# Performance work log

Hardware: AMD Instinct MI355X
Metric: run time of the kernel (lower is better)

The kernel has to match this reference:

```python
import jax, jax.numpy as jnp
import numpy as np

N_NODES = 50000
N_EDGES = 1600000


def _gcn_conv(x, src, dst, W, b, num_nodes):
    # PyG GCNConv: out = D^-1/2 (A + I) D^-1/2 (x W) + b
    h = x @ W  # transform first (in_channels >= out_channels)
    deg = jax.ops.segment_sum(jnp.ones_like(dst, dtype=h.dtype), dst,
                              num_segments=num_nodes)
    dinv = jax.lax.rsqrt(deg)  # deg >= 1 thanks to self-loops
    norm = dinv[src] * dinv[dst]  # [E+N]
    msg = h[src] * norm[:, None]  # gather + scale
    out = jax.ops.segment_sum(msg, dst, num_segments=num_nodes)
    return out + b


def setup_inputs() -> dict:
    key = jax.random.key(0)
    k1, k2, k3, k4 = jax.random.split(key, 4)
    x = jax.random.normal(k1, (N_NODES, 512), dtype=jnp.float32)
    edge_index = jax.random.randint(k2, (2, N_EDGES), 0, N_NODES, dtype=jnp.int64)
    # Glorot-ish init for the two GCNConv weights
    W1 = jax.random.normal(k3, (512, 128), dtype=jnp.float32) * (1.0 / np.sqrt(512))
    b1 = jnp.zeros((128,), dtype=jnp.float32)
    W2 = jax.random.normal(k4, (128, 64), dtype=jnp.float32) * (1.0 / np.sqrt(128))
    b2 = jnp.zeros((64,), dtype=jnp.float32)
    return {"x": x, "edge_index": edge_index, "W1": W1, "b1": b1,
            "W2": W2, "b2": b2}


def reference(x, edge_index, W1, b1, W2, b2):
    num_nodes = x.shape[0]
    loop = jnp.arange(num_nodes, dtype=edge_index.dtype)
    src = jnp.concatenate([edge_index[0], loop])  # add self-loops
    dst = jnp.concatenate([edge_index[1], loop])
    h = jax.nn.relu(_gcn_conv(x, src, dst, W1, b1, num_nodes))
    out = _gcn_conv(h, src, dst, W2, b2, num_nodes)
    return out
```

## Files before the change

### kernel.cpp

```cpp
#include <hip/hip_runtime.h>
#include <hip/hip_bf16.h>


typedef __attribute__((ext_vector_type(8))) short short8;
typedef __attribute__((ext_vector_type(4))) float f32x4;

#define BSHIFT 9
#define BSIZE 512
constexpr int NBMAX = 128;
constexpr int CAP = 32768;
constexpr int CHUNK = 4096;

__device__ __forceinline__ unsigned short bf16_bits(float f) {
  __hip_bfloat16 h = __float2bfloat16(f);
  return *(unsigned short*)&h;
}
__device__ __forceinline__ float bf16_f(unsigned short u) {
  __hip_bfloat16 h = *(__hip_bfloat16*)&u;
  return __bfloat162float(h);
}

__device__ __forceinline__ void gload_lds16(const void* g, void* l) {
  __builtin_amdgcn_global_load_lds(
      (const __attribute__((address_space(1))) unsigned*)g,
      (__attribute__((address_space(3))) unsigned*)l, 16, 0, 0);
}

__device__ __forceinline__ int edge_at(const void* p, long long i, int is64) {
  return is64 ? (int)((const long long*)p)[i] : ((const int*)p)[i];
}

__global__ void k_detect(const int* __restrict__ w, int* flag, int nwords,
                         int* __restrict__ ccur, int NB) {
  __shared__ int nz;
  if (threadIdx.x == 0) nz = 0;
  __syncthreads();
  for (int i = 1 + 2 * (int)threadIdx.x; i < nwords; i += 2 * (int)blockDim.x)
    if (w[i] != 0) nz = 1;
  if ((int)threadIdx.x < NB) ccur[threadIdx.x] = (int)threadIdx.x * CAP;
  __syncthreads();
  if (threadIdx.x == 0) *flag = (nz == 0) ? 1 : 0;
}

__global__ __launch_bounds__(256) void k_binA(
    const void* __restrict__ eidx, const int* __restrict__ flag,
    int* __restrict__ ccur, unsigned* __restrict__ pairs, int E, int NB) {
  __shared__ int cnt[NBMAX];
  __shared__ int scn[NBMAX + 1];
  __shared__ int cur[NBMAX];
  __shared__ int gbase[NBMAX];
  __shared__ unsigned out[CHUNK];
  const int is64 = *flag;
  const int tid = threadIdx.x;
  const int cs = blockIdx.x * CHUNK;
  const int n = min(CHUNK, E - cs);
  for (int b = tid; b < NB; b += 256) cnt[b] = 0;
  __syncthreads();
  unsigned pk[CHUNK / 256];
#pragma unroll
  for (int it = 0; it < CHUNK / 256; ++it) {
    int i = cs + it * 256 + tid;
    unsigned p = 0xFFFFFFFFu;
    if (i < E) {
      int s = edge_at(eidx, i, is64);
      int d = edge_at(eidx, (long long)E + i, is64);
      p = ((unsigned)d << 16) | (unsigned)s;
      atomicAdd(&cnt[d >> BSHIFT], 1);
    }
    pk[it] = p;
  }
  __syncthreads();
  if (tid < NB) scn[tid + 1] = cnt[tid];
  if (tid == 0) scn[0] = 0;
  __syncthreads();
  for (int off = 1; off < NB; off <<= 1) {
    int t = 0;
    if (tid < NB && tid + 1 > off) t = scn[tid + 1 - off];
    __syncthreads();
    if (tid < NB && tid + 1 > off) scn[tid + 1] += t;
    __syncthreads();
  }
  if (tid < NB) {
    cur[tid] = scn[tid];
    gbase[tid] = (cnt[tid] > 0) ? atomicAdd(&ccur[tid], cnt[tid]) : 0;
  }
  __syncthreads();
#pragma unroll
  for (int it = 0; it < CHUNK / 256; ++it) {
    unsigned p = pk[it];
    if (p != 0xFFFFFFFFu) {
      int b = (int)(p >> (16 + BSHIFT));
      int pos = atomicAdd(&cur[b], 1);
      out[pos] = p;
    }
  }
  __syncthreads();
  for (int p2 = tid; p2 < n; p2 += 256) {
    unsigned v = out[p2];
    int b = (int)(v >> (16 + BSHIFT));
    pairs[gbase[b] + (p2 - scn[b])] = v;
  }
}

__global__ __launch_bounds__(128) void k_scanb(
    const int* __restrict__ ccur, int* __restrict__ bbase,
    int* __restrict__ rowptr, int NB, int N, int E) {
  __shared__ int buf[NBMAX];
  int tid = threadIdx.x;
  int v = (tid < NB) ? (ccur[tid] - tid * CAP) : 0;
  buf[tid] = v;
  __syncthreads();
  for (int off = 1; off < NBMAX; off <<= 1) {
    int t = (tid >= off) ? buf[tid - off] : 0;
    __syncthreads();
    buf[tid] += t;
    __syncthreads();
  }
  if (tid < NB) bbase[tid] = buf[tid] - v;
  if (tid == 0) rowptr[N] = E;
}

__global__ __launch_bounds__(256) void k_binB(
    const unsigned* __restrict__ pairs, const int* __restrict__ ccur,
    const int* __restrict__ bbase, int* __restrict__ rowptr,
    float* __restrict__ dinv, int* __restrict__ elist, int N) {
  __shared__ int hist[BSIZE];
  __shared__ int loc[BSIZE];
  const int b = blockIdx.x;
  const int tid = threadIdx.x;
  const int nbeg = b * CAP;
  const int cntb = ccur[b] - nbeg;
  const int base = bbase[b];
  const int j0 = tid, j1 = tid + 256;
  hist[j0] = 0; hist[j1] = 0;
  __syncthreads();
  for (int i = tid; i < cntb; i += 256) {
    unsigned v = pairs[nbeg + i];
    atomicAdd(&hist[(v >> 16) & (BSIZE - 1)], 1);
  }
  __syncthreads();
  loc[j0] = hist[j0]; loc[j1] = hist[j1];
  __syncthreads();
  for (int off = 1; off < BSIZE; off <<= 1) {
    int v0 = (j0 >= off) ? loc[j0 - off] : 0;
    int v1 = (j1 >= off) ? loc[j1 - off] : 0;
    __syncthreads();
    loc[j0] += v0; loc[j1] += v1;
    __syncthreads();
  }
  int c0 = base + loc[j0] - hist[j0];
  int c1 = base + loc[j1] - hist[j1];
  int gd0 = b * BSIZE + j0, gd1 = b * BSIZE + j1;
  if (gd0 < N) { rowptr[gd0] = c0; dinv[gd0] = rsqrtf((float)(hist[j0] + 1)); }
  if (gd1 < N) { rowptr[gd1] = c1; dinv[gd1] = rsqrtf((float)(hist[j1] + 1)); }
  __syncthreads();
  hist[j0] = c0; hist[j1] = c1;
  __syncthreads();
  for (int i = tid; i < cntb; i += 256) {
    unsigned v = pairs[nbeg + i];
    int p = atomicAdd(&hist[(v >> 16) & (BSIZE - 1)], 1);
    elist[p] = (int)(v & 0xFFFFu);
  }
}

__global__ void k_prepw(const float* __restrict__ W, unsigned short* __restrict__ Whi,
                        unsigned short* __restrict__ Wlo, int K, int N) {
  int o = blockIdx.x * blockDim.x + threadIdx.x;
  if (o >= K * N) return;
  int n = o / K, k = o % K;
  float w = W[(long long)k * N + n];
  unsigned short hb = bf16_bits(w);
  unsigned short lb = bf16_bits(w - bf16_f(hb));
  Whi[o] = hb;
  Wlo[o] = lb;
}

template <int K, int NOUT, int WM, int WY, int WX>
__global__ __launch_bounds__(256) void k_gemm_mfma(
    const float* __restrict__ X, const unsigned short* __restrict__ Whi,
    const unsigned short* __restrict__ Wlo, const float* __restrict__ dinv,
    unsigned short* __restrict__ Hs, int M) {
  constexpr int BM = WM * WY;
  constexpr int BN = 64 * WX;
  constexpr int KC = 32;
  constexpr int I = WM / 16;
  static_assert(WY * WX == 4, "4 waves");
  static_assert(BN == NOUT, "block covers full N");
  static_assert((BN * 4) % 256 == 0, "B chunk count divisible by block");
  __shared__ unsigned short Ah[BM][KC], Al[BM][KC];
  __shared__ unsigned short Bh[BN][KC], Bl[BN][KC];
  const int tid = threadIdx.x;
  const int lane = tid & 63, wv = tid >> 6;
  const int wy = wv / WX, wx = wv % WX;
  const int fm = lane & 15;
  const int fq = lane >> 4;
  const int base = blockIdx.x * BM;

  f32x4 acc[I][4];
#pragma unroll
  for (int i = 0; i < I; ++i)
#pragma unroll
    for (int j = 0; j < 4; ++j) acc[i][j] = (f32x4){0.f, 0.f, 0.f, 0.f};

  for (int k0 = 0; k0 < K; k0 += KC) {
    __syncthreads();
#pragma unroll
    for (int it = 0; it < BM / 32; ++it) {
      int chunk = tid + it * 256;
      int r = chunk >> 3, c = chunk & 7;
      float4 v = make_float4(0.f, 0.f, 0.f, 0.f);
      if (base + r < M) v = *(const float4*)&X[(long long)(base + r) * K + k0 + c * 4];
      ushort4 hv, lv;
      hv.x = bf16_bits(v.x); lv.x = bf16_bits(v.x - bf16_f(hv.x));
      hv.y = bf16_bits(v.y); lv.y = bf16_bits(v.y - bf16_f(hv.y));
      hv.z = bf16_bits(v.z); lv.z = bf16_bits(v.z - bf16_f(hv.z));
      hv.w = bf16_bits(v.w); lv.w = bf16_bits(v.w - bf16_f(hv.w));
      *(ushort4*)&Ah[r][c * 4] = hv;
      *(ushort4*)&Al[r][c * 4] = lv;
    }
#pragma unroll
    for (int it = 0; it < (BN * 4) / 256; ++it) {
      int cb = it * 256 + wv * 64;
      int chunk = cb + lane;
      int n = chunk >> 2, cc = chunk & 3;
      const long long go = (long long)n * K + k0 + cc * 8;
      gload_lds16(&Whi[go], (unsigned short*)Bh + (size_t)cb * 8);
      gload_lds16(&Wlo[go], (unsigned short*)Bl + (size_t)cb * 8);
    }
    __syncthreads();
    short8 ah[I], al[I], bh[4], bl[4];
#pragma unroll
    for (int i = 0; i < I; ++i) {
      ah[i] = *(short8*)&Ah[wy * WM + i * 16 + fm][fq * 8];
      al[i] = *(short8*)&Al[wy * WM + i * 16 + fm][fq * 8];
    }
#pragma unroll
    for (int j = 0; j < 4; ++j) {
      bh[j] = *(short8*)&Bh[wx * 64 + j * 16 + fm][fq * 8];
      bl[j] = *(short8*)&Bl[wx * 64 + j * 16 + fm][fq * 8];
    }
#pragma unroll
    for (int i = 0; i < I; ++i)
#pragma unroll
      for (int j = 0; j < 4; ++j) {
        acc[i][j] = __builtin_amdgcn_mfma_f32_16x16x32_bf16(ah[i], bh[j], acc[i][j], 0, 0, 0);
        acc[i][j] = __builtin_amdgcn_mfma_f32_16x16x32_bf16(ah[i], bl[j], acc[i][j], 0, 0, 0);
        acc[i][j] = __builtin_amdgcn_mfma_f32_16x16x32_bf16(al[i], bh[j], acc[i][j], 0, 0, 0);
      }
  }
#pragma unroll
  for (int i = 0; i < I; ++i) {
#pragma unroll
    for (int reg = 0; reg < 4; ++reg) {
      int row = base + wy * WM + i * 16 + fq * 4 + reg;
      if (row < M) {
        float dv = dinv[row];
#pragma unroll
        for (int j = 0; j < 4; ++j)
          Hs[(long long)row * NOUT + wx * 64 + j * 16 + fm] =
              bf16_bits(acc[i][j][reg] * dv);
      }
    }
  }
}

__device__ __forceinline__ void acc8(float* a, uint4 u) {
  const unsigned* p = (const unsigned*)&u;
#pragma unroll
  for (int q = 0; q < 4; ++q) {
    unsigned w = p[q];
    a[2 * q]     += __uint_as_float(w << 16);
    a[2 * q + 1] += __uint_as_float(w & 0xFFFF0000u);
  }
}

template <int C, bool RELU>
__global__ __launch_bounds__(256) void k_gather(
    const int* __restrict__ rowptr, const int* __restrict__ elist,
    const float* __restrict__ dinv, const unsigned short* __restrict__ Hs,
    const float* __restrict__ bias, float* __restrict__ OUT, int N) {
  constexpr int TPN = C / 8;
  constexpr int NPB = 256 / TPN;
  const int node = blockIdx.x * NPB + (int)threadIdx.x / TPN;
  const int lane = (int)threadIdx.x % TPN;
  if (node >= N) return;
  const int col = lane * 8;
  const int beg = rowptr[node];
  const int end = rowptr[node + 1];
  float a0[8] = {0, 0, 0, 0, 0, 0, 0, 0};
  float a1[8] = {0, 0, 0, 0, 0, 0, 0, 0};
  acc8(a0, *(const uint4*)&Hs[(long long)node * C + col]);
  int e = beg;
  for (; e + 3 < end; e += 4) {
    int s0 = elist[e], s1 = elist[e + 1], s2 = elist[e + 2], s3 = elist[e + 3];
    uint4 v0 = *(const uint4*)&Hs[(long long)s0 * C + col];
    uint4 v1 = *(const uint4*)&Hs[(long long)s1 * C + col];
    uint4 v2 = *(const uint4*)&Hs[(long long)s2 * C + col];
    uint4 v3 = *(const uint4*)&Hs[(long long)s3 * C + col];
    acc8(a0, v0); acc8(a1, v1); acc8(a0, v2); acc8(a1, v3);
  }
  for (; e < end; ++e) {
    uint4 v0 = *(const uint4*)&Hs[(long long)elist[e] * C + col];
    acc8(a0, v0);
  }
  const float dv = dinv[node];
  float o[8];
#pragma unroll
  for (int i = 0; i < 8; ++i) {
    o[i] = (a0[i] + a1[i]) * dv + bias[col + i];
    if (RELU) o[i] = fmaxf(o[i], 0.f);
  }
  *(float4*)&OUT[(long long)node * C + col] = make_float4(o[0], o[1], o[2], o[3]);
  *(float4*)&OUT[(long long)node * C + col + 4] = make_float4(o[4], o[5], o[6], o[7]);
}

extern "C" void kernel_launch(void* const* d_in, const int* in_sizes, int n_in,
                              void* d_out, int out_size, void* d_ws, size_t ws_size,
                              hipStream_t stream) {
  const float* x  = (const float*)d_in[0];
  const void*  ei = d_in[1];
  const float* W1 = (const float*)d_in[2];
  const float* b1 = (const float*)d_in[3];
  const float* W2 = (const float*)d_in[4];
  const float* b2 = (const float*)d_in[5];
  float* out = (float*)d_out;
  const int N = in_sizes[0] / 512;
  const int E = in_sizes[1] / 2;
  const int NB = (N + BSIZE - 1) >> BSHIFT;

  char* ws = (char*)d_ws;
  size_t off = 0;
  auto take = [&](size_t bytes) {
    void* p = ws + off;
    off = (off + bytes + 255) & ~(size_t)255;
    return p;
  };
  float* dinv   = (float*)take((size_t)N * 4);
  int*   flag   = (int*)take(4);
  int*   rowptr = (int*)take((size_t)(N + 1) * 4);
  int*   ccur   = (int*)take((size_t)NBMAX * 4);
  int*   bbase  = (int*)take((size_t)NBMAX * 4);
  int*   elist  = (int*)take((size_t)E * 4);
  unsigned short* Wt1h = (unsigned short*)take((size_t)512 * 128 * 2);
  unsigned short* Wt1l = (unsigned short*)take((size_t)512 * 128 * 2);
  unsigned short* Wt2h = (unsigned short*)take((size_t)128 * 64 * 2);
  unsigned short* Wt2l = (unsigned short*)take((size_t)128 * 64 * 2);
  unsigned short* Hs = (unsigned short*)take((size_t)N * 128 * 2);
  float* h2     = (float*)take((size_t)N * 128 * 4);
  unsigned short* Hs2 = Hs;
  unsigned* pairs = (unsigned*)h2;

  const int B = 256;
  k_detect<<<1, B, 0, stream>>>((const int*)ei, flag, 2048, ccur, NB);
  k_binA<<<(E + CHUNK - 1) / CHUNK, B, 0, stream>>>(ei, flag, ccur, pairs, E, NB);
  k_scanb<<<1, 128, 0, stream>>>(ccur, bbase, rowptr, NB, N, E);
  k_binB<<<NB, B, 0, stream>>>(pairs, ccur, bbase, rowptr, dinv, elist, N);
  k_prepw<<<(512 * 128 + B - 1) / B, B, 0, stream>>>(W1, Wt1h, Wt1l, 512, 128);
  k_prepw<<<(128 * 64 + B - 1) / B, B, 0, stream>>>(W2, Wt2h, Wt2l, 128, 64);
  k_gemm_mfma<512, 128, 32, 2, 2><<<(N + 63) / 64, B, 0, stream>>>(
      x, Wt1h, Wt1l, dinv, Hs, N);
  k_gather<128, true><<<(N + 15) / 16, B, 0, stream>>>(rowptr, elist, dinv, Hs, b1, h2, N);
  k_gemm_mfma<128, 64, 32, 4, 1><<<(N + 127) / 128, B, 0, stream>>>(
      h2, Wt2h, Wt2l, dinv, Hs2, N);
  k_gather<64, false><<<(N + 31) / 32, B, 0, stream>>>(rowptr, elist, dinv, Hs2, b2, out, N);
}
```

Measured before the change: 350.5 us.

## Double-buffer MFMA GEMM tiles and merge weight-prep launches

The GEMM kernel now keeps two LDS buffers for the A and B tiles. The next K-chunk's X loads and W global-to-LDS copies are issued before the current chunk's MFMAs, and the bf16 split of A is written to the other buffer afterwards, so only one barrier is needed per iteration. This aims to hide global memory latency behind the matrix math, at the cost of doubled LDS use and extra registers for the prefetched A values, which may lower occupancy. Separately, the two weight-prep launches are merged into one kernel to remove a launch.

Result: no change. 351.6 us (+0.3%).

```diff
diff --git a/kernel.cpp b/kernel.cpp
--- a/kernel.cpp
+++ b/kernel.cpp
@@ -163,16 +163,20 @@
   }
 }
 
-__global__ void k_prepw(const float* __restrict__ W, unsigned short* __restrict__ Whi,
-                        unsigned short* __restrict__ Wlo, int K, int N) {
+__global__ void k_prepw2(const float* __restrict__ W1, unsigned short* __restrict__ W1h,
+                         unsigned short* __restrict__ W1l,
+                         const float* __restrict__ W2, unsigned short* __restrict__ W2h,
+                         unsigned short* __restrict__ W2l) {
   int o = blockIdx.x * blockDim.x + threadIdx.x;
-  if (o >= K * N) return;
+  const float* W; unsigned short *Wh, *Wl; int K, N;
+  if (o < 512 * 128) { W = W1; Wh = W1h; Wl = W1l; K = 512; N = 128; }
+  else { o -= 512 * 128; if (o >= 128 * 64) return; W = W2; Wh = W2h; Wl = W2l; K = 128; N = 64; }
   int n = o / K, k = o % K;
   float w = W[(long long)k * N + n];
   unsigned short hb = bf16_bits(w);
   unsigned short lb = bf16_bits(w - bf16_f(hb));
-  Whi[o] = hb;
-  Wlo[o] = lb;
+  Wh[o] = hb;
+  Wl[o] = lb;
 }
 
 template <int K, int NOUT, int WM, int WY, int WX>
@@ -184,11 +188,12 @@
   constexpr int BN = 64 * WX;
   constexpr int KC = 32;
   constexpr int I = WM / 16;
+  constexpr int AIT = BM / 32;
+  constexpr int BIT = (BN * 4) / 256;
   static_assert(WY * WX == 4, "4 waves");
   static_assert(BN == NOUT, "block covers full N");
-  static_assert((BN * 4) % 256 == 0, "B chunk count divisible by block");
-  __shared__ unsigned short Ah[BM][KC], Al[BM][KC];
-  __shared__ unsigned short Bh[BN][KC], Bl[BN][KC];
+  __shared__ unsigned short Ah[2][BM][KC], Al[2][BM][KC];
+  __shared__ unsigned short Bh[2][BN][KC], Bl[2][BN][KC];
   const int tid = threadIdx.x;
   const int lane = tid & 63, wv = tid >> 6;
   const int wy = wv / WX, wx = wv % WX;
@@ -196,49 +201,74 @@
   const int fq = lane >> 4;
   const int base = blockIdx.x * BM;
 
-  f32x4 acc[I][4];
-#pragma unroll
-  for (int i = 0; i < I; ++i)
-#pragma unroll
-    for (int j = 0; j < 4; ++j) acc[i][j] = (f32x4){0.f, 0.f, 0.f, 0.f};
-
-  for (int k0 = 0; k0 < K; k0 += KC) {
-    __syncthreads();
-#pragma unroll
-    for (int it = 0; it < BM / 32; ++it) {
+  float4 av[AIT];
+
+  auto loadA = [&](int k0) {
+#pragma unroll
+    for (int it = 0; it < AIT; ++it) {
       int chunk = tid + it * 256;
       int r = chunk >> 3, c = chunk & 7;
-      float4 v = make_float4(0.f, 0.f, 0.f, 0.f);
-      if (base + r < M) v = *(const float4*)&X[(long long)(base + r) * K + k0 + c * 4];
+      av[it] = make_float4(0.f, 0.f, 0.f, 0.f);
+      if (base + r < M)
+        av[it] = *(const float4*)&X[(long long)(base + r) * K + k0 + c * 4];
+    }
+  };
+  auto writeA = [&](int buf) {
+#pragma unroll
+    for (int it = 0; it < AIT; ++it) {
+      int chunk = tid + it * 256;
+      int r = chunk >> 3, c = chunk & 7;
+      float4 v = av[it];
       ushort4 hv, lv;
       hv.x = bf16_bits(v.x); lv.x = bf16_bits(v.x - bf16_f(hv.x));
       hv.y = bf16_bits(v.y); lv.y = bf16_bits(v.y - bf16_f(hv.y));
       hv.z = bf16_bits(v.z); lv.z = bf16_bits(v.z - bf16_f(hv.z));
       hv.w = bf16_bits(v.w); lv.w = bf16_bits(v.w - bf16_f(hv.w));
-      *(ushort4*)&Ah[r][c * 4] = hv;
-      *(ushort4*)&Al[r][c * 4] = lv;
-    }
-#pragma unroll
-    for (int it = 0; it < (BN * 4) / 256; ++it) {
+      *(ushort4*)&Ah[buf][r][c * 4] = hv;
+      *(ushort4*)&Al[buf][r][c * 4] = lv;
+    }
+  };
+  auto loadB = [&](int buf, int k0) {
+#pragma unroll
+    for (int it = 0; it < BIT; ++it) {
       int cb = it * 256 + wv * 64;
       int chunk = cb + lane;
       int n = chunk >> 2, cc = chunk & 3;
       const long long go = (long long)n * K + k0 + cc * 8;
-      gload_lds16(&Whi[go], (unsigned short*)Bh + (size_t)cb * 8);
-      gload_lds16(&Wlo[go], (unsigned short*)Bl + (size_t)cb * 8);
-    }
-    __syncthreads();
+      gload_lds16(&Whi[go], (unsigned short*)Bh[buf] + (size_t)cb * 8);
+      gload_lds16(&Wlo[go], (unsigned short*)Bl[buf] + (size_t)cb * 8);
+    }
+  };
+
+  f32x4 acc[I][4];
+#pragma unroll
+  for (int i = 0; i < I; ++i)
+#pragma unroll
+    for (int j = 0; j < 4; ++j) acc[i][j] = (f32x4){0.f, 0.f, 0.f, 0.f};
+
+  loadA(0);
+  loadB(0, 0);
+  writeA(0);
+  __syncthreads();
+
+  constexpr int NIT = K / KC;
+  for (int kk = 0; kk < NIT; ++kk) {
+    const int buf = kk & 1;
+    const int nxt = buf ^ 1;
+    const bool more = (kk + 1) < NIT;
+    if (more) loadB(nxt, (kk + 1) * KC);
     short8 ah[I], al[I], bh[4], bl[4];
 #pragma unroll
     for (int i = 0; i < I; ++i) {
-      ah[i] = *(short8*)&Ah[wy * WM + i * 16 + fm][fq * 8];
-      al[i] = *(short8*)&Al[wy * WM + i * 16 + fm][fq * 8];
+      ah[i] = *(short8*)&Ah[buf][wy * WM + i * 16 + fm][fq * 8];
+      al[i] = *(short8*)&Al[buf][wy * WM + i * 16 + fm][fq * 8];
     }
 #pragma unroll
     for (int j = 0; j < 4; ++j) {
-      bh[j] = *(short8*)&Bh[wx * 64 + j * 16 + fm][fq * 8];
-      bl[j] = *(short8*)&Bl[wx * 64 + j * 16 + fm][fq * 8];
-    }
+      bh[j] = *(short8*)&Bh[buf][wx * 64 + j * 16 + fm][fq * 8];
+      bl[j] = *(short8*)&Bl[buf][wx * 64 + j * 16 + fm][fq * 8];
+    }
+    if (more) loadA((kk + 1) * KC);
 #pragma unroll
     for (int i = 0; i < I; ++i)
 #pragma unroll
@@ -247,6 +277,10 @@
         acc[i][j] = __builtin_amdgcn_mfma_f32_16x16x32_bf16(ah[i], bl[j], acc[i][j], 0, 0, 0);
         acc[i][j] = __builtin_amdgcn_mfma_f32_16x16x32_bf16(al[i], bh[j], acc[i][j], 0, 0, 0);
       }
+    if (more) {
+      writeA(nxt);
+      __syncthreads();
+    }
   }
 #pragma unroll
   for (int i = 0; i < I; ++i) {
@@ -355,8 +389,8 @@
   k_binA<<<(E + CHUNK - 1) / CHUNK, B, 0, stream>>>(ei, flag, ccur, pairs, E, NB);
   k_scanb<<<1, 128, 0, stream>>>(ccur, bbase, rowptr, NB, N, E);
   k_binB<<<NB, B, 0, stream>>>(pairs, ccur, bbase, rowptr, dinv, elist, N);
-  k_prepw<<<(512 * 128 + B - 1) / B, B, 0, stream>>>(W1, Wt1h, Wt1l, 512, 128);
-  k_prepw<<<(128 * 64 + B - 1) / B, B, 0, stream>>>(W2, Wt2h, Wt2l, 128, 64);
+  k_prepw2<<<(512 * 128 + 128 * 64 + B - 1) / B, B, 0, stream>>>(
+      W1, Wt1h, Wt1l, W2, Wt2h, Wt2l);
   k_gemm_mfma<512, 128, 32, 2, 2><<<(N + 63) / 64, B, 0, stream>>>(
       x, Wt1h, Wt1l, dinv, Hs, N);
   k_gather<128, true><<<(N + 15) / 16, B, 0, stream>>>(rowptr, elist, dinv, Hs, b1, h2, N);
```

## Fuse all GCN stages into one persistent cooperative kernel with grid syncs

Applied to the files above, without the earlier changes.

Replaces ten separate kernel launches (detect, binning, scan, CSR build, weight prep, two GEMMs, two gathers) with a single cooperative persistent kernel. Stages are separated by grid.sync() and blocks loop over tiles, chunks and groups. The goal is to remove launch gaps and per-kernel tail effects. In exchange, every phase is capped at a fixed grid size (at most 1536 blocks), shared memory is one 24 KB buffer reused across phases, and grid-wide barriers may cost more than the launch overhead they replace.

New measurement: 760.4 us. 2.17x slower.

```diff
diff --git a/kernel.cpp b/kernel.cpp
--- a/kernel.cpp
+++ b/kernel.cpp
@@ -1,5 +1,8 @@
 #include <hip/hip_runtime.h>
 #include <hip/hip_bf16.h>
+#include <hip/hip_cooperative_groups.h>
+
+namespace cg = cooperative_groups;
 
 
 typedef __attribute__((ext_vector_type(8))) short short8;
@@ -19,182 +22,48 @@
   __hip_bfloat16 h = *(__hip_bfloat16*)&u;
   return __bfloat162float(h);
 }
-
 __device__ __forceinline__ void gload_lds16(const void* g, void* l) {
   __builtin_amdgcn_global_load_lds(
       (const __attribute__((address_space(1))) unsigned*)g,
       (__attribute__((address_space(3))) unsigned*)l, 16, 0, 0);
 }
-
 __device__ __forceinline__ int edge_at(const void* p, long long i, int is64) {
   return is64 ? (int)((const long long*)p)[i] : ((const int*)p)[i];
 }
 
-__global__ void k_detect(const int* __restrict__ w, int* flag, int nwords,
-                         int* __restrict__ ccur, int NB) {
-  __shared__ int nz;
-  if (threadIdx.x == 0) nz = 0;
-  __syncthreads();
-  for (int i = 1 + 2 * (int)threadIdx.x; i < nwords; i += 2 * (int)blockDim.x)
-    if (w[i] != 0) nz = 1;
-  if ((int)threadIdx.x < NB) ccur[threadIdx.x] = (int)threadIdx.x * CAP;
-  __syncthreads();
-  if (threadIdx.x == 0) *flag = (nz == 0) ? 1 : 0;
-}
-
-__global__ __launch_bounds__(256) void k_binA(
-    const void* __restrict__ eidx, const int* __restrict__ flag,
-    int* __restrict__ ccur, unsigned* __restrict__ pairs, int E, int NB) {
-  __shared__ int cnt[NBMAX];
-  __shared__ int scn[NBMAX + 1];
-  __shared__ int cur[NBMAX];
-  __shared__ int gbase[NBMAX];
-  __shared__ unsigned out[CHUNK];
-  const int is64 = *flag;
-  const int tid = threadIdx.x;
-  const int cs = blockIdx.x * CHUNK;
-  const int n = min(CHUNK, E - cs);
-  for (int b = tid; b < NB; b += 256) cnt[b] = 0;
-  __syncthreads();
-  unsigned pk[CHUNK / 256];
-#pragma unroll
-  for (int it = 0; it < CHUNK / 256; ++it) {
-    int i = cs + it * 256 + tid;
-    unsigned p = 0xFFFFFFFFu;
-    if (i < E) {
-      int s = edge_at(eidx, i, is64);
-      int d = edge_at(eidx, (long long)E + i, is64);
-      p = ((unsigned)d << 16) | (unsigned)s;
-      atomicAdd(&cnt[d >> BSHIFT], 1);
-    }
-    pk[it] = p;
-  }
-  __syncthreads();
-  if (tid < NB) scn[tid + 1] = cnt[tid];
-  if (tid == 0) scn[0] = 0;
-  __syncthreads();
-  for (int off = 1; off < NB; off <<= 1) {
-    int t = 0;
-    if (tid < NB && tid + 1 > off) t = scn[tid + 1 - off];
-    __syncthreads();
-    if (tid < NB && tid + 1 > off) scn[tid + 1] += t;
-    __syncthreads();
-  }
-  if (tid < NB) {
-    cur[tid] = scn[tid];
-    gbase[tid] = (cnt[tid] > 0) ? atomicAdd(&ccur[tid], cnt[tid]) : 0;
-  }
-  __syncthreads();
-#pragma unroll
-  for (int it = 0; it < CHUNK / 256; ++it) {
-    unsigned p = pk[it];
-    if (p != 0xFFFFFFFFu) {
-      int b = (int)(p >> (16 + BSHIFT));
-      int pos = atomicAdd(&cur[b], 1);
-      out[pos] = p;
-    }
-  }
-  __syncthreads();
-  for (int p2 = tid; p2 < n; p2 += 256) {
-    unsigned v = out[p2];
-    int b = (int)(v >> (16 + BSHIFT));
-    pairs[gbase[b] + (p2 - scn[b])] = v;
-  }
-}
-
-__global__ __launch_bounds__(128) void k_scanb(
-    const int* __restrict__ ccur, int* __restrict__ bbase,
-    int* __restrict__ rowptr, int NB, int N, int E) {
-  __shared__ int buf[NBMAX];
-  int tid = threadIdx.x;
-  int v = (tid < NB) ? (ccur[tid] - tid * CAP) : 0;
-  buf[tid] = v;
-  __syncthreads();
-  for (int off = 1; off < NBMAX; off <<= 1) {
-    int t = (tid >= off) ? buf[tid - off] : 0;
-    __syncthreads();
-    buf[tid] += t;
-    __syncthreads();
-  }
-  if (tid < NB) bbase[tid] = buf[tid] - v;
-  if (tid == 0) rowptr[N] = E;
-}
-
-__global__ __launch_bounds__(256) void k_binB(
-    const unsigned* __restrict__ pairs, const int* __restrict__ ccur,
-    const int* __restrict__ bbase, int* __restrict__ rowptr,
-    float* __restrict__ dinv, int* __restrict__ elist, int N) {
-  __shared__ int hist[BSIZE];
-  __shared__ int loc[BSIZE];
-  const int b = blockIdx.x;
-  const int tid = threadIdx.x;
-  const int nbeg = b * CAP;
-  const int cntb = ccur[b] - nbeg;
-  const int base = bbase[b];
-  const int j0 = tid, j1 = tid + 256;
-  hist[j0] = 0; hist[j1] = 0;
-  __syncthreads();
-  for (int i = tid; i < cntb; i += 256) {
-    unsigned v = pairs[nbeg + i];
-    atomicAdd(&hist[(v >> 16) & (BSIZE - 1)], 1);
-  }
-  __syncthreads();
-  loc[j0] = hist[j0]; loc[j1] = hist[j1];
-  __syncthreads();
-  for (int off = 1; off < BSIZE; off <<= 1) {
-    int v0 = (j0 >= off) ? loc[j0 - off] : 0;
-    int v1 = (j1 >= off) ? loc[j1 - off] : 0;
-    __syncthreads();
-    loc[j0] += v0; loc[j1] += v1;
-    __syncthreads();
-  }
-  int c0 = base + loc[j0] - hist[j0];
-  int c1 = base + loc[j1] - hist[j1];
-  int gd0 = b * BSIZE + j0, gd1 = b * BSIZE + j1;
-  if (gd0 < N) { rowptr[gd0] = c0; dinv[gd0] = rsqrtf((float)(hist[j0] + 1)); }
-  if (gd1 < N) { rowptr[gd1] = c1; dinv[gd1] = rsqrtf((float)(hist[j1] + 1)); }
-  __syncthreads();
-  hist[j0] = c0; hist[j1] = c1;
-  __syncthreads();
-  for (int i = tid; i < cntb; i += 256) {
-    unsigned v = pairs[nbeg + i];
-    int p = atomicAdd(&hist[(v >> 16) & (BSIZE - 1)], 1);
-    elist[p] = (int)(v & 0xFFFFu);
-  }
-}
-
-__global__ void k_prepw(const float* __restrict__ W, unsigned short* __restrict__ Whi,
-                        unsigned short* __restrict__ Wlo, int K, int N) {
-  int o = blockIdx.x * blockDim.x + threadIdx.x;
-  if (o >= K * N) return;
-  int n = o / K, k = o % K;
-  float w = W[(long long)k * N + n];
-  unsigned short hb = bf16_bits(w);
-  unsigned short lb = bf16_bits(w - bf16_f(hb));
-  Whi[o] = hb;
-  Wlo[o] = lb;
-}
+struct GcnParams {
+  const float* x; const void* ei;
+  const float* W1; const float* b1; const float* W2; const float* b2;
+  float* out;
+  int N, E, NB, nchunks;
+  int* flag; int* ccur; int* rowptr; float* dinv; int* elist;
+  unsigned* pairs;
+  unsigned short *W1h, *W1l, *W2h, *W2l;
+  unsigned short* Hs;
+  float* h2;
+};
 
 template <int K, int NOUT, int WM, int WY, int WX>
-__global__ __launch_bounds__(256) void k_gemm_mfma(
+__device__ __forceinline__ void gemm_tile(
     const float* __restrict__ X, const unsigned short* __restrict__ Whi,
     const unsigned short* __restrict__ Wlo, const float* __restrict__ dinv,
-    unsigned short* __restrict__ Hs, int M) {
+    unsigned short* __restrict__ Hs, int M, int tile, char* smem) {
   constexpr int BM = WM * WY;
   constexpr int BN = 64 * WX;
   constexpr int KC = 32;
   constexpr int I = WM / 16;
   static_assert(WY * WX == 4, "4 waves");
-  static_assert(BN == NOUT, "block covers full N");
-  static_assert((BN * 4) % 256 == 0, "B chunk count divisible by block");
-  __shared__ unsigned short Ah[BM][KC], Al[BM][KC];
-  __shared__ unsigned short Bh[BN][KC], Bl[BN][KC];
+  static_assert((BM + BM + BN + BN) * KC * 2 <= 24576, "fits smem");
+  unsigned short* Ah = (unsigned short*)smem;
+  unsigned short* Al = Ah + BM * KC;
+  unsigned short* Bh = Al + BM * KC;
+  unsigned short* Bl = Bh + BN * KC;
   const int tid = threadIdx.x;
   const int lane = tid & 63, wv = tid >> 6;
   const int wy = wv / WX, wx = wv % WX;
   const int fm = lane & 15;
   const int fq = lane >> 4;
-  const int base = blockIdx.x * BM;
+  const int base = tile * BM;
 
   f32x4 acc[I][4];
 #pragma unroll
@@ -215,8 +84,8 @@
       hv.y = bf16_bits(v.y); lv.y = bf16_bits(v.y - bf16_f(hv.y));
       hv.z = bf16_bits(v.z); lv.z = bf16_bits(v.z - bf16_f(hv.z));
       hv.w = bf16_bits(v.w); lv.w = bf16_bits(v.w - bf16_f(hv.w));
-      *(ushort4*)&Ah[r][c * 4] = hv;
-      *(ushort4*)&Al[r][c * 4] = lv;
+      *(ushort4*)&Ah[r * KC + c * 4] = hv;
+      *(ushort4*)&Al[r * KC + c * 4] = lv;
     }
 #pragma unroll
     for (int it = 0; it < (BN * 4) / 256; ++it) {
@@ -224,20 +93,20 @@
       int chunk = cb + lane;
       int n = chunk >> 2, cc = chunk & 3;
       const long long go = (long long)n * K + k0 + cc * 8;
-      gload_lds16(&Whi[go], (unsigned short*)Bh + (size_t)cb * 8);
-      gload_lds16(&Wlo[go], (unsigned short*)Bl + (size_t)cb * 8);
+      gload_lds16(&Whi[go], Bh + (size_t)cb * 8);
+      gload_lds16(&Wlo[go], Bl + (size_t)cb * 8);
     }
     __syncthreads();
     short8 ah[I], al[I], bh[4], bl[4];
 #pragma unroll
     for (int i = 0; i < I; ++i) {
-      ah[i] = *(short8*)&Ah[wy * WM + i * 16 + fm][fq * 8];
-      al[i] = *(short8*)&Al[wy * WM + i * 16 + fm][fq * 8];
+      ah[i] = *(short8*)&Ah[(wy * WM + i * 16 + fm) * KC + fq * 8];
+      al[i] = *(short8*)&Al[(wy * WM + i * 16 + fm) * KC + fq * 8];
     }
 #pragma unroll
     for (int j = 0; j < 4; ++j) {
-      bh[j] = *(short8*)&Bh[wx * 64 + j * 16 + fm][fq * 8];
-      bl[j] = *(short8*)&Bl[wx * 64 + j * 16 + fm][fq * 8];
+      bh[j] = *(short8*)&Bh[(wx * 64 + j * 16 + fm) * KC + fq * 8];
+      bl[j] = *(short8*)&Bl[(wx * 64 + j * 16 + fm) * KC + fq * 8];
     }
 #pragma unroll
     for (int i = 0; i < I; ++i)
@@ -275,13 +144,13 @@
 }
 
 template <int C, bool RELU>
-__global__ __launch_bounds__(256) void k_gather(
+__device__ __forceinline__ void gather_grp(
     const int* __restrict__ rowptr, const int* __restrict__ elist,
     const float* __restrict__ dinv, const unsigned short* __restrict__ Hs,
-    const float* __restrict__ bias, float* __restrict__ OUT, int N) {
+    const float* __restrict__ bias, float* __restrict__ OUT, int N, int g) {
   constexpr int TPN = C / 8;
   constexpr int NPB = 256 / TPN;
-  const int node = blockIdx.x * NPB + (int)threadIdx.x / TPN;
+  const int node = g * NPB + (int)threadIdx.x / TPN;
   const int lane = (int)threadIdx.x % TPN;
   if (node >= N) return;
   const int col = lane * 8;
@@ -314,53 +183,224 @@
   *(float4*)&OUT[(long long)node * C + col + 4] = make_float4(o[4], o[5], o[6], o[7]);
 }
 
+__global__ __launch_bounds__(256, 4) void k_fused(GcnParams p) {
+  cg::grid_group grid = cg::this_grid();
+  __shared__ __align__(16) char smem[24576];
+  const int tid = threadIdx.x;
+  const int bid = blockIdx.x;
+  const int nb = gridDim.x;
+
+  if (bid == 0) {
+    int* s = (int*)smem;
+    if (tid == 0) s[0] = 0;
+    __syncthreads();
+    int nz = 0;
+    for (int i = 1 + 2 * tid; i < 4096; i += 512)
+      nz |= (((const int*)p.ei)[i] != 0);
+    if (nz) s[0] = 1;
+    if (tid < NBMAX) p.ccur[tid] = 0;
+    __syncthreads();
+    if (tid == 0) *p.flag = (s[0] == 0) ? 1 : 0;
+  }
+  {
+    constexpr int JT = (512 * 128 + 128 * 64) / 256;
+    for (int j = bid; j < JT; j += nb) {
+      int o = j * 256 + tid;
+      const float* W; unsigned short *Wh, *Wl; int K, Nn;
+      if (o < 512 * 128) { W = p.W1; Wh = p.W1h; Wl = p.W1l; K = 512; Nn = 128; }
+      else { o -= 512 * 128; W = p.W2; Wh = p.W2h; Wl = p.W2l; K = 128; Nn = 64; }
+      int n = o / K, k = o % K;
+      float w = W[(long long)k * Nn + n];
+      unsigned short hb = bf16_bits(w);
+      Wh[o] = hb;
+      Wl[o] = bf16_bits(w - bf16_f(hb));
+    }
+  }
+  grid.sync();
+
+  {
+    const int is64 = *p.flag;
+    int* cnt = (int*)smem;
+    int* scn = cnt + NBMAX;
+    int* cur = scn + NBMAX + 4;
+    int* gbase = cur + NBMAX;
+    unsigned* out = (unsigned*)(smem + 4096);
+    for (int c = bid; c < p.nchunks; c += nb) {
+      const int cs = c * CHUNK;
+      const int n = min(CHUNK, p.E - cs);
+      for (int b = tid; b < NBMAX; b += 256) cnt[b] = 0;
+      __syncthreads();
+      unsigned pk[CHUNK / 256];
+#pragma unroll
+      for (int it = 0; it < CHUNK / 256; ++it) {
+        int i = cs + it * 256 + tid;
+        unsigned pe = 0xFFFFFFFFu;
+        if (i < p.E) {
+          int s = edge_at(p.ei, i, is64);
+          int d = edge_at(p.ei, (long long)p.E + i, is64);
+          pe = ((unsigned)d << 16) | (unsigned)s;
+          atomicAdd(&cnt[d >> BSHIFT], 1);
+        }
+        pk[it] = pe;
+      }
+      __syncthreads();
+      if (tid < p.NB) scn[tid + 1] = cnt[tid];
+      if (tid == 0) scn[0] = 0;
+      __syncthreads();
+      for (int off = 1; off < p.NB; off <<= 1) {
+        int t = 0;
+        if (tid < p.NB && tid + 1 > off) t = scn[tid + 1 - off];
+        __syncthreads();
+        if (tid < p.NB && tid + 1 > off) scn[tid + 1] += t;
+        __syncthreads();
+      }
+      if (tid < p.NB) {
+        cur[tid] = scn[tid];
+        gbase[tid] = (cnt[tid] > 0)
+            ? (tid * CAP + atomicAdd(&p.ccur[tid], cnt[tid])) : 0;
+      }
+      __syncthreads();
+#pragma unroll
+      for (int it = 0; it < CHUNK / 256; ++it) {
+        unsigned pe = pk[it];
+        if (pe != 0xFFFFFFFFu) {
+          int b = (int)(pe >> (16 + BSHIFT));
+          int pos = atomicAdd(&cur[b], 1);
+          out[pos] = pe;
+        }
+      }
+      __syncthreads();
+      for (int p2 = tid; p2 < n; p2 += 256) {
+        unsigned v = out[p2];
+        int b = (int)(v >> (16 + BSHIFT));
+        p.pairs[gbase[b] + (p2 - scn[b])] = v;
+      }
+    }
+  }
+  grid.sync();
+
+  if (bid == 0 && tid == 0) p.rowptr[p.N] = p.E;
+  if (bid < p.NB) {
+    int* scn2 = (int*)smem;
+    int* hist = (int*)(smem + 1024);
+    int* loc  = (int*)(smem + 1024 + 2048);
+    if (tid < NBMAX) scn2[tid] = (tid < p.NB) ? p.ccur[tid] : 0;
+    __syncthreads();
+    for (int off = 1; off < NBMAX; off <<= 1) {
+      int t = (tid < NBMAX && tid >= off) ? scn2[tid - off] : 0;
+      __syncthreads();
+      if (tid < NBMAX) scn2[tid] += t;
+      __syncthreads();
+    }
+    const int cntb = p.ccur[bid];
+    const int base = scn2[bid] - cntb;
+    const int nbeg = bid * CAP;
+    const int j0 = tid, j1 = tid + 256;
+    hist[j0] = 0; hist[j1] = 0;
+    __syncthreads();
+    for (int i = tid; i < cntb; i += 256) {
+      unsigned v = p.pairs[nbeg + i];
+      atomicAdd(&hist[(v >> 16) & (BSIZE - 1)], 1);
+    }
+    __syncthreads();
+    loc[j0] = hist[j0]; loc[j1] = hist[j1];
+    __syncthreads();
+    for (int off = 1; off < BSIZE; off <<= 1) {
+      int v0 = (j0 >= off) ? loc[j0 - off] : 0;
+      int v1 = (j1 >= off) ? loc[j1 - off] : 0;
+      __syncthreads();
+      loc[j0] += v0; loc[j1] += v1;
+      __syncthreads();
+    }
+    int c0 = base + loc[j0] - hist[j0];
+    int c1 = base + loc[j1] - hist[j1];
+    int gd0 = bid * BSIZE + j0, gd1 = bid * BSIZE + j1;
+    if (gd0 < p.N) { p.rowptr[gd0] = c0; p.dinv[gd0] = rsqrtf((float)(hist[j0] + 1)); }
+    if (gd1 < p.N) { p.rowptr[gd1] = c1; p.dinv[gd1] = rsqrtf((float)(hist[j1] + 1)); }
+    __syncthreads();
+    hist[j0] = c0; hist[j1] = c1;
+    __syncthreads();
+    for (int i = tid; i < cntb; i += 256) {
+      unsigned v = p.pairs[nbeg + i];
+      int pos = atomicAdd(&hist[(v >> 16) & (BSIZE - 1)], 1);
+      p.elist[pos] = (int)(v & 0xFFFFu);
+    }
+  }
+  grid.sync();
+
+  {
+    const int nt = (p.N + 63) / 64;
+    for (int t = bid; t < nt; t += nb)
+      gemm_tile<512, 128, 32, 2, 2>(p.x, p.W1h, p.W1l, p.dinv, p.Hs, p.N, t, smem);
+  }
+  grid.sync();
+
+  {
+    const int ng = (p.N + 15) / 16;
+    for (int g = bid; g < ng; g += nb)
+      gather_grp<128, true>(p.rowptr, p.elist, p.dinv, p.Hs, p.b1, p.h2, p.N, g);
+  }
+  grid.sync();
+
+  {
+    const int nt = (p.N + 127) / 128;
+    for (int t = bid; t < nt; t += nb)
+      gemm_tile<128, 64, 32, 4, 1>(p.h2, p.W2h, p.W2l, p.dinv, p.Hs, p.N, t, smem);
+  }
+  grid.sync();
+
+  {
+    const int ng = (p.N + 31) / 32;
+    for (int g = bid; g < ng; g += nb)
+      gather_grp<64, false>(p.rowptr, p.elist, p.dinv, p.Hs, p.b2, p.out, p.N, g);
+  }
+}
+
 extern "C" void kernel_launch(void* const* d_in, const int* in_sizes, int n_in,
                               void* d_out, int out_size, void* d_ws, size_t ws_size,
                               hipStream_t stream) {
-  const float* x  = (const float*)d_in[0];
-  const void*  ei = d_in[1];
-  const float* W1 = (const float*)d_in[2];
-  const float* b1 = (const float*)d_in[3];
-  const float* W2 = (const float*)d_in[4];
-  const float* b2 = (const float*)d_in[5];
-  float* out = (float*)d_out;
   const int N = in_sizes[0] / 512;
   const int E = in_sizes[1] / 2;
-  const int NB = (N + BSIZE - 1) >> BSHIFT;
 
   char* ws = (char*)d_ws;
   size_t off = 0;
   auto take = [&](size_t bytes) {
-    void* p = ws + off;
+    void* ptr = ws + off;
     off = (off + bytes + 255) & ~(size_t)255;
-    return p;
+    return ptr;
   };
-  float* dinv   = (float*)take((size_t)N * 4);
-  int*   flag   = (int*)take(4);
-  int*   rowptr = (int*)take((size_t)(N + 1) * 4);
-  int*   ccur   = (int*)take((size_t)NBMAX * 4);
-  int*   bbase  = (int*)take((size_t)NBMAX * 4);
-  int*   elist  = (int*)take((size_t)E * 4);
-  unsigned short* Wt1h = (unsigned short*)take((size_t)512 * 128 * 2);
-  unsigned short* Wt1l = (unsigned short*)take((size_t)512 * 128 * 2);
-  unsigned short* Wt2h = (unsigned short*)take((size_t)128 * 64 * 2);
-  unsigned short* Wt2l = (unsigned short*)take((size_t)128 * 64 * 2);
-  unsigned short* Hs = (unsigned short*)take((size_t)N * 128 * 2);
-  float* h2     = (float*)take((size_t)N * 128 * 4);
-  unsigned short* Hs2 = Hs;
-  unsigned* pairs = (unsigned*)h2;
-
-  const int B = 256;
-  k_detect<<<1, B, 0, stream>>>((const int*)ei, flag, 2048, ccur, NB);
-  k_binA<<<(E + CHUNK - 1) / CHUNK, B, 0, stream>>>(ei, flag, ccur, pairs, E, NB);
-  k_scanb<<<1, 128, 0, stream>>>(ccur, bbase, rowptr, NB, N, E);
-  k_binB<<<NB, B, 0, stream>>>(pairs, ccur, bbase, rowptr, dinv, elist, N);
-  k_prepw<<<(512 * 128 + B - 1) / B, B, 0, stream>>>(W1, Wt1h, Wt1l, 512, 128);
-  k_prepw<<<(128 * 64 + B - 1) / B, B, 0, stream>>>(W2, Wt2h, Wt2l, 128, 64);
-  k_gemm_mfma<512, 128, 32, 2, 2><<<(N + 63) / 64, B, 0, stream>>>(
-      x, Wt1h, Wt1l, dinv, Hs, N);
-  k_gather<128, true><<<(N + 15) / 16, B, 0, stream>>>(rowptr, elist, dinv, Hs, b1, h2, N);
-  k_gemm_mfma<128, 64, 32, 4, 1><<<(N + 127) / 128, B, 0, stream>>>(
-      h2, Wt2h, Wt2l, dinv, Hs2, N);
-  k_gather<64, false><<<(N + 31) / 32, B, 0, stream>>>(rowptr, elist, dinv, Hs2, b2, out, N);
-}
+  GcnParams p;
+  p.x  = (const float*)d_in[0];
+  p.ei = d_in[1];
+  p.W1 = (const float*)d_in[2];
+  p.b1 = (const float*)d_in[3];
+  p.W2 = (const float*)d_in[4];
+  p.b2 = (const float*)d_in[5];
+  p.out = (float*)d_out;
+  p.N = N;
+  p.E = E;
+  p.NB = (N + BSIZE - 1) >> BSHIFT;
+  p.nchunks = (E + CHUNK - 1) / CHUNK;
+  p.dinv   = (float*)take((size_t)N * 4);
+  p.flag   = (int*)take(4);
+  p.rowptr = (int*)take((size_t)(N + 1) * 4);
+  p.ccur   = (int*)take((size_t)NBMAX * 4);
+  p.elist  = (int*)take((size_t)E * 4);
+  p.W1h = (unsigned short*)take((size_t)512 * 128 * 2);
+  p.W1l = (unsigned short*)take((size_t)512 * 128 * 2);
+  p.W2h = (unsigned short*)take((size_t)128 * 64 * 2);
+  p.W2l = (unsigned short*)take((size_t)128 * 64 * 2);
+  p.Hs  = (unsigned short*)take((size_t)N * 128 * 2);
+  p.h2  = (float*)take((size_t)N * 128 * 4);
+  p.pairs = (unsigned*)p.h2;
+
+  int maxb = 4;
+  hipOccupancyMaxActiveBlocksPerMultiprocessor(&maxb, k_fused, 256, 0);
+  if (maxb < 1) maxb = 1;
+  long long g = (long long)maxb * 256;
+  if (g > 1536) g = 1536;
+  if (g < 256) g = 256;
+  void* args[] = {(void*)&p};
+  hipLaunchCooperativeKernel((const void*)k_fused, dim3((unsigned)g), dim3(256),
+                             args, 0, stream);
+}
```
